# Kernel optimization log

Measured on AMD Instinct MI355X. Metric: run time of the kernel, lower is better.

## Reference

```python
import jax, jax.numpy as jnp
import numpy as np

B, T, D = 16, 4096, 768
S_MAX = 128  # max sentence (segment) count per sample


def setup_inputs() -> dict:
    key = jax.random.key(0)
    ks = jax.random.split(key, 8)
    hidden = jax.random.normal(ks[0], (B, T, D), dtype=jnp.float32)
    # sorted per-token segment ids == cumulative torch.split span structure
    seg_ids = jnp.sort(jax.random.randint(ks[1], (B, T), 0, S_MAX, dtype=jnp.int32), axis=-1)
    s1, s2, s3 = 1.0 / np.sqrt(D), 1.0 / np.sqrt(384), 1.0 / np.sqrt(128)
    W1 = jax.random.normal(ks[2], (D, 384), dtype=jnp.float32) * s1
    b1 = jnp.zeros((384,), dtype=jnp.float32)
    W2 = jax.random.normal(ks[3], (384, 128), dtype=jnp.float32) * s2
    b2 = jnp.zeros((128,), dtype=jnp.float32)
    W3 = jax.random.normal(ks[4], (128, 2), dtype=jnp.float32) * s3
    b3 = jnp.zeros((2,), dtype=jnp.float32)
    return {"hidden": hidden, "seg_ids": seg_ids, "W1": W1, "b1": b1,
            "W2": W2, "b2": b2, "W3": W3, "b3": b3}


def reference(hidden, seg_ids, W1, b1, W2, b2, W3, b3):
    # split_tensor: per-sample segment-sum over token spans, padded to S_MAX.
    # Segments with no tokens come out zero, matching F.pad of the torch code.
    sent_em = jax.vmap(
        lambda h, s: jax.ops.segment_sum(h, s, num_segments=S_MAX)
    )(hidden, seg_ids)  # [B, S_MAX, D]
    # sent_pred MLP head
    x = jax.nn.relu(jnp.einsum('bsd,df->bsf', sent_em, W1) + b1)
    x = jax.nn.relu(jnp.einsum('bsf,fg->bsg', x, W2) + b2)
    pred = jnp.einsum('bsg,gc->bsc', x, W3) + b3  # [B, S_MAX, 2]
    return pred.reshape(B * S_MAX, -1)
```

## Files before the change

### kernel.cpp

```cpp
#include <hip/hip_runtime.h>

#define BATCH 16
#define TOK   4096
#define DIM   768
#define SMAX  128
#define BM    8

__device__ __forceinline__ int lower_bound_i(const int* __restrict__ a, int n, int v) {
    int lo = 0, hi = n;
    while (lo < hi) {
        int m = (lo + hi) >> 1;
        if (a[m] < v) lo = m + 1; else hi = m;
    }
    return lo;
}

__device__ __forceinline__ float f4get(const float4& v, int k) {
    switch (k) {
        case 0: return v.x;
        case 1: return v.y;
        case 2: return v.z;
        default: return v.w;
    }
}

__device__ __forceinline__ void f4acc(float4& a, const float4& v) {
    a.x += v.x; a.y += v.y; a.z += v.z; a.w += v.w;
}

__global__ __launch_bounds__(192)
void bounds_kernel(const int* __restrict__ seg, int* __restrict__ bounds) {
    const int b = blockIdx.x;
    const int s = threadIdx.x;
    if (s <= SMAX)
        bounds[b * (SMAX + 1) + s] = lower_bound_i(seg + b * TOK, TOK, s);
}

__global__ __launch_bounds__(192)
void segsum_kernel(const float* __restrict__ hidden,
                   const int* __restrict__ bounds,
                   float* __restrict__ sent) {
    const int s = blockIdx.x;
    const int b = blockIdx.y;
    const int tid = threadIdx.x;

    const int lo = bounds[b * (SMAX + 1) + s];
    const int hi = bounds[b * (SMAX + 1) + s + 1];

    const float4* __restrict__ hp =
        reinterpret_cast<const float4*>(hidden + (size_t)b * TOK * DIM) + tid;

    float4 acc = make_float4(0.f, 0.f, 0.f, 0.f);
    int t = lo;

    for (; t + 16 <= hi; t += 16) {
        float4 v[16];
        #pragma unroll
        for (int u = 0; u < 16; ++u)
            v[u] = hp[(size_t)(t + u) * (DIM / 4)];
        #pragma unroll
        for (int u = 0; u < 16; ++u)
            f4acc(acc, v[u]);
    }
    for (; t + 4 <= hi; t += 4) {
        float4 v[4];
        #pragma unroll
        for (int u = 0; u < 4; ++u)
            v[u] = hp[(size_t)(t + u) * (DIM / 4)];
        #pragma unroll
        for (int u = 0; u < 4; ++u)
            f4acc(acc, v[u]);
    }
    for (; t < hi; ++t)
        f4acc(acc, hp[(size_t)t * (DIM / 4)]);

    float4* outp = reinterpret_cast<float4*>(sent + (size_t)(b * SMAX + s) * DIM);
    outp[tid] = acc;
}

__global__ __launch_bounds__(1024)
void mlp_kernel(const float* __restrict__ sent,
                const float* __restrict__ W1, const float* __restrict__ b1,
                const float* __restrict__ W2, const float* __restrict__ b2,
                const float* __restrict__ W3, const float* __restrict__ b3,
                float* __restrict__ out) {
    __shared__ __align__(16) float A [BM * DIM];
    __shared__ __align__(16) float X1[BM * 384];
    __shared__ __align__(16) float X2[BM * 128];
    __shared__ __align__(16) float P [8 * BM * 384];

    const int tid  = threadIdx.x;
    const int row0 = blockIdx.x * BM;
    const int c1   = tid & 127;
    const int kg   = tid >> 7;

    {
        const float4* sA = reinterpret_cast<const float4*>(sent + (size_t)row0 * DIM);
        float4* dA = reinterpret_cast<float4*>(A);
        for (int i = tid; i < BM * DIM / 4; i += 1024)
            dA[i] = sA[i];
    }
    __syncthreads();

    {
        float acc[BM][3];
        #pragma unroll
        for (int r = 0; r < BM; ++r)
            #pragma unroll
            for (int j = 0; j < 3; ++j) acc[r][j] = 0.f;

        const int k0 = kg * 96;
        for (int k = k0; k < k0 + 96; k += 4) {
            float4 a[BM];
            #pragma unroll
            for (int r = 0; r < BM; ++r)
                a[r] = *reinterpret_cast<const float4*>(&A[r * DIM + k]);
            #pragma unroll
            for (int kk = 0; kk < 4; ++kk) {
                const float w0 = W1[(size_t)(k + kk) * 384 + c1];
                const float w1 = W1[(size_t)(k + kk) * 384 + c1 + 128];
                const float w2 = W1[(size_t)(k + kk) * 384 + c1 + 256];
                #pragma unroll
                for (int r = 0; r < BM; ++r) {
                    const float av = f4get(a[r], kk);
                    acc[r][0] = fmaf(av, w0, acc[r][0]);
                    acc[r][1] = fmaf(av, w1, acc[r][1]);
                    acc[r][2] = fmaf(av, w2, acc[r][2]);
                }
            }
        }
        #pragma unroll
        for (int r = 0; r < BM; ++r)
            #pragma unroll
            for (int j = 0; j < 3; ++j)
                P[(kg * BM + r) * 384 + c1 + j * 128] = acc[r][j];
    }
    __syncthreads();

    for (int i = tid; i < BM * 384; i += 1024) {
        const int row = i / 384;
        const int col = i - row * 384;
        float s = b1[col];
        #pragma unroll
        for (int g = 0; g < 8; ++g)
            s += P[(g * BM + row) * 384 + col];
        X1[i] = s > 0.f ? s : 0.f;
    }
    __syncthreads();

    {
        float acc2[BM];
        #pragma unroll
        for (int r = 0; r < BM; ++r) acc2[r] = 0.f;

        const int k0 = kg * 48;
        for (int k = k0; k < k0 + 48; k += 4) {
            float4 x[BM];
            #pragma unroll
            for (int r = 0; r < BM; ++r)
                x[r] = *reinterpret_cast<const float4*>(&X1[r * 384 + k]);
            #pragma unroll
            for (int kk = 0; kk < 4; ++kk) {
                const float w = W2[(size_t)(k + kk) * 128 + c1];
                #pragma unroll
                for (int r = 0; r < BM; ++r)
                    acc2[r] = fmaf(f4get(x[r], kk), w, acc2[r]);
            }
        }
        #pragma unroll
        for (int r = 0; r < BM; ++r)
            P[(kg * BM + r) * 128 + c1] = acc2[r];
    }
    __syncthreads();

    {
        const int row = tid >> 7;
        const int col = c1;
        float s = b2[col];
        #pragma unroll
        for (int g = 0; g < 8; ++g)
            s += P[(g * BM + row) * 128 + col];
        X2[row * 128 + col] = s > 0.f ? s : 0.f;
    }
    __syncthreads();

    if (tid < BM * 2) {
        const int r = tid >> 1;
        const int c = tid & 1;
        float sacc = 0.f;
        #pragma unroll 8
        for (int k = 0; k < 128; ++k)
            sacc = fmaf(X2[r * 128 + k], W3[k * 2 + c], sacc);
        out[(row0 + r) * 2 + c] = sacc + b3[c];
    }
}

extern "C" void kernel_launch(void* const* d_in, const int* in_sizes, int n_in,
                              void* d_out, int out_size, void* d_ws, size_t ws_size,
                              hipStream_t stream) {
    const float* hidden = (const float*)d_in[0];
    const int*   seg    = (const int*)d_in[1];
    const float* W1     = (const float*)d_in[2];
    const float* b1     = (const float*)d_in[3];
    const float* W2     = (const float*)d_in[4];
    const float* b2     = (const float*)d_in[5];
    const float* W3     = (const float*)d_in[6];
    const float* b3     = (const float*)d_in[7];
    float* out  = (float*)d_out;
    float* sent = (float*)d_ws;

    const size_t sent_bytes = (size_t)BATCH * SMAX * DIM * sizeof(float);
    const size_t bounds_bytes = (size_t)BATCH * (SMAX + 1) * sizeof(int);
    int* bounds;
    if (ws_size >= sent_bytes + bounds_bytes)
        bounds = (int*)((char*)d_ws + sent_bytes);
    else
        bounds = (int*)d_out;

    bounds_kernel<<<BATCH, 192, 0, stream>>>(seg, bounds);
    segsum_kernel<<<dim3(SMAX, BATCH), 192, 0, stream>>>(hidden, bounds, sent);
    mlp_kernel<<<(BATCH * SMAX) / BM, 1024, 0, stream>>>(sent, W1, b1, W2, b2, W3, b3, out);
}
```

Baseline: 72.94 us.

## Fuse segment-sum into MLP kernel, removing intermediate sentence buffer

Folds the per-segment token reduction into the MLP kernel. Each 128-thread group sums one of the block's 8 segments straight into shared memory using float2 loads, and the separate segsum kernel and its global sentence buffer are removed. This drops one launch plus the write and read of a 6 MB intermediate. In exchange the hidden-state reads now run in only 256 blocks of 1024 threads instead of 2048 small blocks, which may lower memory-level parallelism for the dominant streaming read.

```diff
diff --git a/kernel.cpp b/kernel.cpp
--- a/kernel.cpp
+++ b/kernel.cpp
@@ -24,8 +24,8 @@
     }
 }
 
-__device__ __forceinline__ void f4acc(float4& a, const float4& v) {
-    a.x += v.x; a.y += v.y; a.z += v.z; a.w += v.w;
+__device__ __forceinline__ void f2acc(float2& a, const float2& v) {
+    a.x += v.x; a.y += v.y;
 }
 
 __global__ __launch_bounds__(192)
@@ -36,54 +36,13 @@
         bounds[b * (SMAX + 1) + s] = lower_bound_i(seg + b * TOK, TOK, s);
 }
 
-__global__ __launch_bounds__(192)
-void segsum_kernel(const float* __restrict__ hidden,
-                   const int* __restrict__ bounds,
-                   float* __restrict__ sent) {
-    const int s = blockIdx.x;
-    const int b = blockIdx.y;
-    const int tid = threadIdx.x;
-
-    const int lo = bounds[b * (SMAX + 1) + s];
-    const int hi = bounds[b * (SMAX + 1) + s + 1];
-
-    const float4* __restrict__ hp =
-        reinterpret_cast<const float4*>(hidden + (size_t)b * TOK * DIM) + tid;
-
-    float4 acc = make_float4(0.f, 0.f, 0.f, 0.f);
-    int t = lo;
-
-    for (; t + 16 <= hi; t += 16) {
-        float4 v[16];
-        #pragma unroll
-        for (int u = 0; u < 16; ++u)
-            v[u] = hp[(size_t)(t + u) * (DIM / 4)];
-        #pragma unroll
-        for (int u = 0; u < 16; ++u)
-            f4acc(acc, v[u]);
-    }
-    for (; t + 4 <= hi; t += 4) {
-        float4 v[4];
-        #pragma unroll
-        for (int u = 0; u < 4; ++u)
-            v[u] = hp[(size_t)(t + u) * (DIM / 4)];
-        #pragma unroll
-        for (int u = 0; u < 4; ++u)
-            f4acc(acc, v[u]);
-    }
-    for (; t < hi; ++t)
-        f4acc(acc, hp[(size_t)t * (DIM / 4)]);
-
-    float4* outp = reinterpret_cast<float4*>(sent + (size_t)(b * SMAX + s) * DIM);
-    outp[tid] = acc;
-}
-
 __global__ __launch_bounds__(1024)
-void mlp_kernel(const float* __restrict__ sent,
-                const float* __restrict__ W1, const float* __restrict__ b1,
-                const float* __restrict__ W2, const float* __restrict__ b2,
-                const float* __restrict__ W3, const float* __restrict__ b3,
-                float* __restrict__ out) {
+void fused_kernel(const float* __restrict__ hidden,
+                  const int* __restrict__ bounds,
+                  const float* __restrict__ W1, const float* __restrict__ b1,
+                  const float* __restrict__ W2, const float* __restrict__ b2,
+                  const float* __restrict__ W3, const float* __restrict__ b3,
+                  float* __restrict__ out) {
     __shared__ __align__(16) float A [BM * DIM];
     __shared__ __align__(16) float X1[BM * 384];
     __shared__ __align__(16) float X2[BM * 128];
@@ -91,16 +50,60 @@
 
     const int tid  = threadIdx.x;
     const int row0 = blockIdx.x * BM;
-    const int c1   = tid & 127;
-    const int kg   = tid >> 7;
-
-    {
-        const float4* sA = reinterpret_cast<const float4*>(sent + (size_t)row0 * DIM);
-        float4* dA = reinterpret_cast<float4*>(A);
-        for (int i = tid; i < BM * DIM / 4; i += 1024)
-            dA[i] = sA[i];
-    }
-    __syncthreads();
+    const int b    = row0 / SMAX;
+    const int s0   = row0 % SMAX;
+
+    {
+        const int grp  = tid >> 7;
+        const int lane = tid & 127;
+
+        const int lo = bounds[b * (SMAX + 1) + s0 + grp];
+        const int hi = bounds[b * (SMAX + 1) + s0 + grp + 1];
+
+        const float2* __restrict__ hp =
+            reinterpret_cast<const float2*>(hidden + (size_t)b * TOK * DIM) + lane * 3;
+
+        float2 a0 = make_float2(0.f, 0.f);
+        float2 a1 = make_float2(0.f, 0.f);
+        float2 a2 = make_float2(0.f, 0.f);
+
+        int t = lo;
+        for (; t + 12 <= hi; t += 12) {
+            float2 v0[12], v1[12], v2[12];
+            #pragma unroll
+            for (int u = 0; u < 12; ++u) {
+                const float2* p = hp + (size_t)(t + u) * 384;
+                v0[u] = p[0]; v1[u] = p[1]; v2[u] = p[2];
+            }
+            #pragma unroll
+            for (int u = 0; u < 12; ++u) {
+                f2acc(a0, v0[u]); f2acc(a1, v1[u]); f2acc(a2, v2[u]);
+            }
+        }
+        for (; t + 4 <= hi; t += 4) {
+            float2 v0[4], v1[4], v2[4];
+            #pragma unroll
+            for (int u = 0; u < 4; ++u) {
+                const float2* p = hp + (size_t)(t + u) * 384;
+                v0[u] = p[0]; v1[u] = p[1]; v2[u] = p[2];
+            }
+            #pragma unroll
+            for (int u = 0; u < 4; ++u) {
+                f2acc(a0, v0[u]); f2acc(a1, v1[u]); f2acc(a2, v2[u]);
+            }
+        }
+        for (; t < hi; ++t) {
+            const float2* p = hp + (size_t)t * 384;
+            f2acc(a0, p[0]); f2acc(a1, p[1]); f2acc(a2, p[2]);
+        }
+
+        float2* dA = reinterpret_cast<float2*>(&A[grp * DIM + lane * 6]);
+        dA[0] = a0; dA[1] = a1; dA[2] = a2;
+    }
+    __syncthreads();
+
+    const int c1 = tid & 127;
+    const int kg = tid >> 7;
 
     {
         float acc[BM][3];
@@ -207,17 +210,9 @@
     const float* W3     = (const float*)d_in[6];
     const float* b3     = (const float*)d_in[7];
     float* out  = (float*)d_out;
-    float* sent = (float*)d_ws;
-
-    const size_t sent_bytes = (size_t)BATCH * SMAX * DIM * sizeof(float);
-    const size_t bounds_bytes = (size_t)BATCH * (SMAX + 1) * sizeof(int);
-    int* bounds;
-    if (ws_size >= sent_bytes + bounds_bytes)
-        bounds = (int*)((char*)d_ws + sent_bytes);
-    else
-        bounds = (int*)d_out;
+    int* bounds = (int*)d_ws;
 
     bounds_kernel<<<BATCH, 192, 0, stream>>>(seg, bounds);
-    segsum_kernel<<<dim3(SMAX, BATCH), 192, 0, stream>>>(hidden, bounds, sent);
-    mlp_kernel<<<(BATCH * SMAX) / BM, 1024, 0, stream>>>(sent, W1, b1, W2, b2, W3, b3, out);
-}
+    fused_kernel<<<(BATCH * SMAX) / BM, 1024, 0, stream>>>(
+        hidden, bounds, W1, b1, W2, b2, W3, b3, out);
+}
```

Result: faster. 67.43 us (-7.6%).
